# Performance work log

Measured on AMD Instinct MI355X. Metric: run time of the kernel, lower is better.

Reference implementation:

```python
import jax, jax.numpy as jnp
import numpy as np

INP = 512
HIDDEN = 512
N_HEADS = 8          # called 'head_dim' in the torch code
D_HEAD = HIDDEN // N_HEADS  # 64
BASE = 10000.0
SCALE = D_HEAD ** (-0.5)


def rope(x):
    # x: [b, s, h, d]
    b, s, h, d = x.shape
    half = d // 2
    theta = 1.0 / (BASE ** (jnp.arange(0, d, 2, dtype=jnp.float32) / d))  # [d/2]
    idx_theta = jnp.arange(s, dtype=jnp.float32)[:, None] * theta[None, :]  # [s, d/2]
    idx_theta2 = jnp.concatenate([idx_theta, idx_theta], axis=1)            # [s, d]
    neg_half = jnp.concatenate([-x[..., half:], x[..., :half]], axis=-1)
    cos = jnp.cos(idx_theta2)[None, :, None, :]
    sin = jnp.sin(idx_theta2)[None, :, None, :]
    return x * cos + neg_half * sin


def setup_inputs() -> dict:
    key = jax.random.key(0)
    ks = jax.random.split(key, 10)
    b, s = 4, 2048
    init = lambda k, shp, fan_in: jax.random.normal(k, shp, jnp.float32) * (fan_in ** -0.5)
    return {
        "x": jax.random.normal(ks[0], (b, s, INP), jnp.float32),
        "c": jax.random.normal(ks[1], (b, s, INP), jnp.float32),
        "Wq": init(ks[2], (INP, HIDDEN), INP), "bq": jnp.zeros((HIDDEN,), jnp.float32),
        "Wk": init(ks[3], (INP, HIDDEN), INP), "bk": jnp.zeros((HIDDEN,), jnp.float32),
        "Wv": init(ks[4], (INP, HIDDEN), INP), "bv": jnp.zeros((HIDDEN,), jnp.float32),
        "Wo": init(ks[5], (HIDDEN, INP), HIDDEN), "bo": jnp.zeros((INP,), jnp.float32),
    }


def reference(x, c, Wq, bq, Wk, bk, Wv, bv, Wo, bo):
    b, s, _ = x.shape
    h_res = x
    q = (c @ Wq + bq).reshape(b, s, N_HEADS, D_HEAD)
    k = (x @ Wk + bk).reshape(b, s, N_HEADS, D_HEAD)
    v = (x @ Wv + bv).reshape(b, s, N_HEADS, D_HEAD)
    q = rope(q)
    k = rope(k)  # computed but unused, exactly as in the source
    # NOTE: source computes scores between q and V (not k) -- faithful reproduction
    att = jnp.einsum('bihd,bjhd->bhij', q, v)            # [b, h, s, s]
    att = jax.nn.softmax(att * SCALE, axis=-1)
    out = jnp.einsum('bhij,bjhd->bihd', att, v)          # [b, s, h, d]
    out = out.reshape(b, s, HIDDEN)
    out = out @ Wo + bo
    return out + h_res
```

## Files before the change

### kernel.cpp

```cpp
#include <hip/hip_runtime.h>
#include <hip/hip_bf16.h>
#include <cstdint>

typedef float f32x4 __attribute__((ext_vector_type(4)));
typedef float f32x16 __attribute__((ext_vector_type(16)));
typedef short bf16x8 __attribute__((ext_vector_type(8)));
typedef short bf16x4 __attribute__((ext_vector_type(4)));
typedef unsigned int u32x2 __attribute__((ext_vector_type(2)));
typedef unsigned short u16;

#define B_    4
#define S_    2048
#define H_    8
#define D_    64
#define M_    8192

#define OFF_CBF   0UL
#define OFF_XBF   8388608UL
#define OFF_QBH   16777216UL
#define OFF_VBH   25165824UL
#define OFF_VTBH  33554432UL
#define OFF_ATTN  41943040UL
#define OFF_WQT   50331648UL
#define OFF_WVT   50855936UL
#define OFF_WOT   51380224UL
#define OFF_BIAS  51904512UL
#define OFF_COS   51910656UL
#define OFF_SIN   52172800UL
#define WS_NEEDED 52434944UL

__device__ __forceinline__ u16 f2bf(float f){
    union { float f; uint32_t u; } v; v.f = f;
    uint32_t r = (v.u + 0x7fffu + ((v.u >> 16) & 1u)) >> 16;
    return (u16)r;
}
__device__ __forceinline__ float bf2f(u16 h){
    union { uint32_t u; float f; } v; v.u = ((uint32_t)h) << 16;
    return v.f;
}

__device__ __forceinline__ uint32_t cvtpk(float lo, float hi){
    uint32_t r;
    asm("v_cvt_pk_bf16_f32 %0, %1, %2" : "=v"(r) : "v"(lo), "v"(hi));
    return r;
}
__device__ __forceinline__ void plswap(uint32_t &va, uint32_t &vb){
#if __has_builtin(__builtin_amdgcn_permlane32_swap)
    u32x2 r = __builtin_amdgcn_permlane32_swap(va, vb, false, false);
    va = r[0]; vb = r[1];
#else
    asm volatile("v_permlane32_swap_b32 %0, %1" : "+v"(va), "+v"(vb));
#endif
}

__device__ __forceinline__ int swz(int row, int col){
    return (col & ~63) | ((((col >> 3) & 7) ^ (row & 7)) << 3) | (col & 7);
}

__device__ __forceinline__ int detect_f32(const void* x_in){
    int lane = threadIdx.x & 63;
    ushort2 dv = ((const ushort2*)x_in)[lane];
    bool hit = ((((dv.x >> 7) & 0xFF) >= 160) || (((dv.y >> 7) & 0xFF) >= 160));
    return __ballot(hit) != 0ULL;
}

__device__ __forceinline__ void gload_lds16(const u16* g, u16* l){
    __builtin_amdgcn_global_load_lds(
        (const __attribute__((address_space(1))) void*)g,
        (__attribute__((address_space(3))) void*)l, 16, 0, 0);
}

__global__ void k_prep(const void* c_in, const void* x_in,
                       const void* Wq, const void* Wv, const void* Wo,
                       const void* bq, const void* bv, const void* bo,
                       u16* c_bf, u16* x_bf,
                       u16* Wqt, u16* Wvt, u16* Wot, float* bias_ws,
                       float* cos_t, float* sin_t){
    int bid = blockIdx.x;
    if (bid >= 11264){
        int idx = (bid - 11264) * 256 + threadIdx.x;
        int pos = idx >> 5, j = idx & 31;
        double theta = pow(10000.0, -(double)j / 32.0);
        double rev = ((double)pos * theta) * 0.15915494309189535;
        rev -= floor(rev);
        float fr = (float)rev;
        cos_t[idx] = __builtin_amdgcn_cosf(fr);
        sin_t[idx] = __builtin_amdgcn_sinf(fr);
        return;
    }
    if (bid >= 8192){
        int f = detect_f32(x_in);
        int wi = (bid - 8192) >> 10;
        int idx = ((bid - 8192) & 1023) * 256 + threadIdx.x;
        int k = idx >> 9, n = idx & 511;
        const void* W; u16* Wt; const void* bb;
        if (wi == 0){ W = Wq; Wt = Wqt; bb = bq; }
        else if (wi == 1){ W = Wv; Wt = Wvt; bb = bv; }
        else { W = Wo; Wt = Wot; bb = bo; }
        float v = f ? ((const float*)W)[idx] : bf2f(((const u16*)W)[idx]);
        Wt[n * 512 + (wi == 2 ? k : swz(n, k))] = f2bf(v);
        if (idx < 512){
            float b = f ? ((const float*)bb)[idx] : bf2f(((const u16*)bb)[idx]);
            bias_ws[wi * 512 + idx] = b;
        }
        return;
    }
    int f = detect_f32(x_in);
    int isx = bid >= 4096;
    int t = (bid & 4095) * 256 + threadIdx.x;
    const void* src = isx ? x_in : c_in;
    u16* dst = isx ? x_bf : c_bf;
    int e0 = t * 4, row = e0 >> 9, col = e0 & 511;
    size_t didx = (size_t)row * 512 + swz(row, col);
    ushort4 o;
    if (f){
        float4 v = ((const float4*)src)[t];
        o.x = f2bf(v.x); o.y = f2bf(v.y); o.z = f2bf(v.z); o.w = f2bf(v.w);
    } else {
        o = ((const ushort4*)src)[t];
    }
    *(ushort4*)(dst + didx) = o;
}

__global__ __launch_bounds__(256) void k_gemm_qv(
    const u16* __restrict__ c_bf, const u16* __restrict__ x_bf,
    const u16* __restrict__ Wqt, const u16* __restrict__ Wvt,
    const float* __restrict__ bias_ws,
    const float* __restrict__ cos_t, const float* __restrict__ sin_t,
    u16* __restrict__ Qbh, u16* __restrict__ Vbh, u16* __restrict__ Vtbh)
{
    __shared__ __align__(16) u16 Als[2][128 * 64];
    __shared__ __align__(16) u16 Bls[2][128 * 64];
    const int w = threadIdx.x >> 6, lane = threadIdx.x & 63;
    const int g = lane >> 4, cq = lane & 15;
    const int wm = w & 1, wn = w >> 1;
    const int z = blockIdx.z;
    const u16* A  = z ? x_bf : c_bf;
    const u16* Wt = z ? Wvt : Wqt;
    const float* bias = bias_ws + (z ? 512 : 0);
    const int m0b = blockIdx.x * 128, n0b = blockIdx.y * 128;
    const int m0 = m0b + wm * 64, n0 = n0b + wn * 64;
    const int swzi = ((cq & 7) << 3);

    int srow[4], scol[4];
    #pragma unroll
    for (int i = 0; i < 4; i++){
        int flat = (w * 4 + i) * 64 + lane;
        srow[i] = flat >> 3; scol[i] = (flat & 7) * 8;
    }

    const f32x4 zero = {0.f, 0.f, 0.f, 0.f};
    f32x4 acc[4][4];
    #pragma unroll
    for (int i = 0; i < 4; i++)
        #pragma unroll
        for (int j = 0; j < 4; j++) acc[i][j] = zero;

    #pragma unroll
    for (int i = 0; i < 4; i++){
        gload_lds16(A  + (size_t)(m0b + srow[i]) * 512 + scol[i], &Als[0][(w*4 + i) * 512]);
        gload_lds16(Wt + (size_t)(n0b + srow[i]) * 512 + scol[i], &Bls[0][(w*4 + i) * 512]);
    }

    for (int kt = 0; kt < 8; kt++){
        const int buf = kt & 1;
        __builtin_amdgcn_s_waitcnt(0x0F70);
        __syncthreads();
        if (kt < 7){
            const int kk = (kt + 1) * 64;
            #pragma unroll
            for (int i = 0; i < 4; i++){
                gload_lds16(A  + (size_t)(m0b + srow[i]) * 512 + kk + scol[i], &Als[buf^1][(w*4 + i) * 512]);
                gload_lds16(Wt + (size_t)(n0b + srow[i]) * 512 + kk + scol[i], &Bls[buf^1][(w*4 + i) * 512]);
            }
        }
        #pragma unroll
        for (int ks = 0; ks < 2; ks++){
            const int cs = ((ks * 4 + g) << 3) ^ swzi;
            bf16x8 a[4], b[4];
            #pragma unroll
            for (int mt = 0; mt < 4; mt++)
                a[mt] = *(const bf16x8*)&Als[buf][(wm*64 + mt*16 + cq) * 64 + cs];
            #pragma unroll
            for (int nt = 0; nt < 4; nt++)
                b[nt] = *(const bf16x8*)&Bls[buf][(wn*64 + nt*16 + cq) * 64 + cs];
            #pragma unroll
            for (int mt = 0; mt < 4; mt++)
                #pragma unroll
                for (int nt = 0; nt < 4; nt++)
                    acc[mt][nt] = __builtin_amdgcn_mfma_f32_16x16x32_bf16(a[mt], b[nt], acc[mt][nt], 0, 0, 0);
        }
    }
    __syncthreads();

    #pragma unroll
    for (int nt = 0; nt < 4; nt++){
        float bvv = bias[n0 + nt*16 + cq];
        #pragma unroll
        for (int mt = 0; mt < 4; mt++) acc[mt][nt] += bvv;
    }
    const int h = n0 >> 6;
    if (z == 0){
        const float SCL = 0.125f * 1.4426950408889634f;
        #pragma unroll
        for (int mt = 0; mt < 4; mt++){
            #pragma unroll
            for (int r = 0; r < 4; r++){
                int row = m0 + mt*16 + g*4 + r;
                int b_idx = row >> 11, si = row & 2047;
                size_t base = ((size_t)(b_idx*8 + h) * 2048 + si) * 64;
                #pragma unroll
                for (int nt = 0; nt < 2; nt++){
                    int dj = nt*16 + cq;
                    float cv = cos_t[si*32 + dj], sv = sin_t[si*32 + dj];
                    float x1 = acc[mt][nt][r], x2 = acc[mt][nt+2][r];
                    Qbh[base + dj]      = f2bf((x1*cv - x2*sv) * SCL);
                    Qbh[base + dj + 32] = f2bf((x2*cv + x1*sv) * SCL);
                }
            }
        }
    } else {
        float* ltw = ((float*)&Als[0][0]) + w * (16 * 65);
        const int b_idx = m0 >> 11, si0 = m0 & 2047;
        const size_t tbase = ((size_t)(b_idx*8 + h) * 64) * 2048;
        #pragma unroll
        for (int mt = 0; mt < 4; mt++)
            #pragma unroll
            for (int r = 0; r < 4; r++){
                int row = m0 + mt*16 + g*4 + r;
                int bi = row >> 11, si = row & 2047;
                size_t base = ((size_t)(bi*8 + h) * 2048 + si) * 64;
                #pragma unroll
                for (int nt = 0; nt < 4; nt++)
                    Vbh[base + nt*16 + cq] = f2bf(acc[mt][nt][r]);
            }
        #pragma unroll
        for (int nt = 0; nt < 4; nt++){
            #pragma unroll
            for (int mt = 0; mt < 4; mt++)
                #pragma unroll
                for (int r = 0; r < 4; r++)
                    ltw[cq * 65 + mt*16 + g*4 + r] = acc[mt][nt][r];
            __builtin_amdgcn_wave_barrier();
            #pragma unroll
            for (int dd = 0; dd < 16; dd++){
                float v = ltw[dd * 65 + lane];
                Vtbh[tbase + (size_t)(nt*16 + dd) * 2048 + si0 + lane] = f2bf(v);
            }
            __builtin_amdgcn_wave_barrier();
        }
    }
}

__global__ __launch_bounds__(256, 4) void k_attn(
    const u16* __restrict__ Qbh, const u16* __restrict__ Vbh,
    const u16* __restrict__ Vtbh,
    u16* __restrict__ part0, u16* __restrict__ part1, float* __restrict__ lsum)
{
    __shared__ __align__(16) u16 Vs[2][64 * 68];
    __shared__ __align__(16) u16 Vts[2][64 * 68];

    const int bid = blockIdx.x;
    const int logical = (bid & 7) * 128 + (bid >> 3);
    const int xb = logical & 15;
    const int bh = (logical >> 4) & 31;
    const int z  = logical >> 9;

    const int w = threadIdx.x >> 6, lane = threadIdx.x & 63;
    const int r32 = lane & 31, hl = lane >> 5;
    const int i0 = xb * 128 + w * 32;
    const int j0 = z * 1024;

    bf16x8 aq[4];
    #pragma unroll
    for (int kk = 0; kk < 4; kk++)
        aq[kk] = *(const bf16x8*)(Qbh + ((size_t)bh*2048 + i0 + r32)*64 + kk*16 + hl*8);

    const int sr = w * 16 + (lane >> 2), sc = (lane & 3) * 16;
    const u16* gvs = Vbh  + ((size_t)bh*2048 + j0 + sr) * 64 + sc;
    const u16* gvt = Vtbh + ((size_t)bh*64 + sr) * 2048 + j0 + sc;
    const int ls = sr * 68 + sc;

    {
        bf16x8 a0 = *(const bf16x8*)gvs,       a1 = *(const bf16x8*)(gvs + 8);
        bf16x8 b0 = *(const bf16x8*)gvt,       b1 = *(const bf16x8*)(gvt + 8);
        *(bf16x8*)&Vs[0][ls]  = a0;  *(bf16x8*)&Vs[0][ls + 8]  = a1;
        *(bf16x8*)&Vts[0][ls] = b0;  *(bf16x8*)&Vts[0][ls + 8] = b1;
    }

    f32x16 ot0 = {0.f,0.f,0.f,0.f,0.f,0.f,0.f,0.f,0.f,0.f,0.f,0.f,0.f,0.f,0.f,0.f};
    f32x16 ot1 = ot0;
    const f32x16 zero16 = ot0;
    float fl = 0.f;

    for (int jt = 0; jt < 16; jt++){
        const int buf = jt & 1;
        __syncthreads();
        bf16x8 na0, na1, nb0, nb1;
        if (jt < 15){
            na0 = *(const bf16x8*)(gvs + (size_t)(jt + 1) * 4096);
            na1 = *(const bf16x8*)(gvs + (size_t)(jt + 1) * 4096 + 8);
            nb0 = *(const bf16x8*)(gvt + (size_t)(jt + 1) * 64);
            nb1 = *(const bf16x8*)(gvt + (size_t)(jt + 1) * 64 + 8);
        }
        bf16x8 pb[4];
        #pragma unroll
        for (int jtile = 0; jtile < 2; jtile++){
            f32x16 st = zero16;
            __builtin_amdgcn_s_setprio(1);
            #pragma unroll
            for (int kk = 0; kk < 4; kk++){
                bf16x8 av = *(const bf16x8*)&Vs[buf][(jtile*32 + r32)*68 + kk*16 + hl*8];
                st = __builtin_amdgcn_mfma_f32_32x32x16_bf16(av, aq[kk], st, 0, 0, 0);
            }
            __builtin_amdgcn_s_setprio(0);
            #pragma unroll
            for (int rr = 0; rr < 16; rr++) st[rr] = __builtin_amdgcn_exp2f(st[rr]);
            {
                float t0 = (st[0]+st[1]) + (st[2]+st[3]);
                float t1 = (st[4]+st[5]) + (st[6]+st[7]);
                float t2 = (st[8]+st[9]) + (st[10]+st[11]);
                float t3 = (st[12]+st[13]) + (st[14]+st[15]);
                fl += (t0+t1) + (t2+t3);
            }
            #pragma unroll
            for (int c = 0; c < 2; c++){
                uint32_t dA1 = cvtpk(st[c*8+0], st[c*8+1]);
                uint32_t dA2 = cvtpk(st[c*8+2], st[c*8+3]);
                uint32_t dB1 = cvtpk(st[c*8+4], st[c*8+5]);
                uint32_t dB2 = cvtpk(st[c*8+6], st[c*8+7]);
                plswap(dA1, dB1);
                plswap(dA2, dB2);
                union { bf16x8 v; uint32_t d[4]; } u;
                u.d[0] = dA1; u.d[1] = dA2; u.d[2] = dB1; u.d[3] = dB2;
                pb[jtile*2 + c] = u.v;
            }
        }
        __builtin_amdgcn_s_setprio(1);
        #pragma unroll
        for (int c = 0; c < 4; c++){
            bf16x8 vt0 = *(const bf16x8*)&Vts[buf][r32*68 + c*16 + hl*8];
            bf16x8 vt1 = *(const bf16x8*)&Vts[buf][(32 + r32)*68 + c*16 + hl*8];
            ot0 = __builtin_amdgcn_mfma_f32_32x32x16_bf16(vt0, pb[c], ot0, 0, 0, 0);
            ot1 = __builtin_amdgcn_mfma_f32_32x32x16_bf16(vt1, pb[c], ot1, 0, 0, 0);
        }
        __builtin_amdgcn_s_setprio(0);
        if (jt < 15){
            *(bf16x8*)&Vs[buf^1][ls]  = na0;  *(bf16x8*)&Vs[buf^1][ls + 8]  = na1;
            *(bf16x8*)&Vts[buf^1][ls] = nb0;  *(bf16x8*)&Vts[buf^1][ls + 8] = nb1;
        }
    }
    const int b_idx = bh >> 3, hh = bh & 7;
    u16* part = z ? part1 : part0;
    float sum = fl + __shfl_xor(fl, 32);
    const int row = b_idx*2048 + i0 + r32;
    if (lane < 32)
        lsum[(size_t)z*65536 + (size_t)hh*8192 + row] = sum;
    #pragma unroll
    for (int dt = 0; dt < 2; dt++){
        #pragma unroll
        for (int q = 0; q < 4; q++){
            float v0 = dt ? ot1[q*4+0] : ot0[q*4+0];
            float v1 = dt ? ot1[q*4+1] : ot0[q*4+1];
            float v2 = dt ? ot1[q*4+2] : ot0[q*4+2];
            float v3 = dt ? ot1[q*4+3] : ot0[q*4+3];
            uint2 pw;
            pw.x = cvtpk(v0, v1);
            pw.y = cvtpk(v2, v3);
            int col = hh*64 + dt*32 + q*8 + hl*4;
            *(uint2*)&part[(size_t)row * 512 + col] = pw;
        }
    }
}

__global__ __launch_bounds__(256) void k_gemm_out(
    const u16* __restrict__ part0, const u16* __restrict__ part1,
    const float* __restrict__ lsum,
    const u16* __restrict__ Wot, const float* __restrict__ bias_ws,
    const void* __restrict__ x_in, void* __restrict__ out)
{
    __shared__ __align__(16) u16 Als[2][128 * 68];
    __shared__ __align__(16) u16 Bls[2][64 * 68];
    const int w = threadIdx.x >> 6, lane = threadIdx.x & 63;
    const int g = lane >> 4, cq = lane & 15;
    const int wm = w & 1, wn = w >> 1;
    const int m0b = blockIdx.x * 128, n0b = blockIdx.y * 64;
    const int m0 = m0b + wm * 64, n0 = n0b + wn * 32;
    const int f = detect_f32(x_in);

    int sra[4], sca[4], srb[2], scb[2];
    #pragma unroll
    for (int i = 0; i < 4; i++){
        int flat = (w * 4 + i) * 64 + lane;
        sra[i] = flat >> 3; sca[i] = (flat & 7) * 8;
    }
    #pragma unroll
    for (int i = 0; i < 2; i++){
        int flat = (w * 2 + i) * 64 + lane;
        srb[i] = flat >> 3; scb[i] = (flat & 7) * 8;
    }

    const f32x4 zero = {0.f, 0.f, 0.f, 0.f};
    f32x4 acc[4][2];
    #pragma unroll
    for (int i = 0; i < 4; i++)
        #pragma unroll
        for (int j = 0; j < 2; j++) acc[i][j] = zero;

    bf16x8 pa0[4], pa1[4], pb[2]; float pr[4];
    #pragma unroll
    for (int i = 0; i < 4; i++){
        int row = m0b + sra[i];
        pa0[i] = *(const bf16x8*)&part0[(size_t)row * 512 + sca[i]];
        pa1[i] = *(const bf16x8*)&part1[(size_t)row * 512 + sca[i]];
        pr[i] = 1.f / (lsum[row] + lsum[65536 + row]);
    }
    #pragma unroll
    for (int i = 0; i < 2; i++)
        pb[i] = *(const bf16x8*)&Wot[(size_t)(n0b + srb[i]) * 512 + scb[i]];
    #pragma unroll
    for (int i = 0; i < 4; i++){
        union { bf16x8 v; u16 e[8]; } a8;
        #pragma unroll
        for (int e = 0; e < 8; e++)
            a8.e[e] = f2bf((bf2f((u16)pa0[i][e]) + bf2f((u16)pa1[i][e])) * pr[i]);
        *(bf16x8*)&Als[0][sra[i]*68 + sca[i]] = a8.v;
    }
    #pragma unroll
    for (int i = 0; i < 2; i++)
        *(bf16x8*)&Bls[0][srb[i]*68 + scb[i]] = pb[i];

    for (int kt = 0; kt < 8; kt++){
        const int buf = kt & 1;
        __syncthreads();
        if (kt < 7){
            const int kk = (kt + 1) * 64, h = kt + 1;
            #pragma unroll
            for (int i = 0; i < 4; i++){
                int row = m0b + sra[i];
                pa0[i] = *(const bf16x8*)&part0[(size_t)row * 512 + kk + sca[i]];
                pa1[i] = *(const bf16x8*)&part1[(size_t)row * 512 + kk + sca[i]];
                pr[i] = 1.f / (lsum[(size_t)h*8192 + row] + lsum[65536 + (size_t)h*8192 + row]);
            }
            #pragma unroll
            for (int i = 0; i < 2; i++)
                pb[i] = *(const bf16x8*)&Wot[(size_t)(n0b + srb[i]) * 512 + kk + scb[i]];
        }
        #pragma unroll
        for (int ks = 0; ks < 2; ks++){
            bf16x8 a[4], b[2];
            #pragma unroll
            for (int mt = 0; mt < 4; mt++)
                a[mt] = *(const bf16x8*)&Als[buf][(wm*64 + mt*16 + cq)*68 + ks*32 + g*8];
            #pragma unroll
            for (int nt = 0; nt < 2; nt++)
                b[nt] = *(const bf16x8*)&Bls[buf][(wn*32 + nt*16 + cq)*68 + ks*32 + g*8];
            #pragma unroll
            for (int mt = 0; mt < 4; mt++)
                #pragma unroll
                for (int nt = 0; nt < 2; nt++)
                    acc[mt][nt] = __builtin_amdgcn_mfma_f32_16x16x32_bf16(a[mt], b[nt], acc[mt][nt], 0, 0, 0);
        }
        if (kt < 7){
            #pragma unroll
            for (int i = 0; i < 4; i++){
                union { bf16x8 v; u16 e[8]; } a8;
                #pragma unroll
                for (int e = 0; e < 8; e++)
                    a8.e[e] = f2bf((bf2f((u16)pa0[i][e]) + bf2f((u16)pa1[i][e])) * pr[i]);
                *(bf16x8*)&Als[buf^1][sra[i]*68 + sca[i]] = a8.v;
            }
            #pragma unroll
            for (int i = 0; i < 2; i++)
                *(bf16x8*)&Bls[buf^1][srb[i]*68 + scb[i]] = pb[i];
        }
    }
    #pragma unroll
    for (int mt = 0; mt < 4; mt++)
        #pragma unroll
        for (int nt = 0; nt < 2; nt++)
            #pragma unroll
            for (int r = 0; r < 4; r++){
                int row = m0 + mt*16 + g*4 + r;
                int col = n0 + nt*16 + cq;
                size_t idx = (size_t)row * 512 + col;
                float resid = f ? ((const float*)x_in)[idx] : bf2f(((const u16*)x_in)[idx]);
                float v = acc[mt][nt][r] + bias_ws[1024 + col] + resid;
                if (f) ((float*)out)[idx] = v;
                else   ((u16*)out)[idx] = f2bf(v);
            }
}

extern "C" void kernel_launch(void* const* d_in, const int* in_sizes, int n_in,
                              void* d_out, int out_size, void* d_ws, size_t ws_size,
                              hipStream_t stream){
    const void* x_in = d_in[0];
    const void* c_in = d_in[1];
    const void* Wq = d_in[2]; const void* bq = d_in[3];
    const void* Wv = d_in[6]; const void* bv = d_in[7];
    const void* Wo = d_in[8]; const void* bo = d_in[9];

    if (ws_size < WS_NEEDED){
        hipMemsetAsync(d_out, 0, (size_t)out_size * 2, stream);
        return;
    }
    char* ws = (char*)d_ws;
    u16* c_bf  = (u16*)(ws + OFF_CBF);
    u16* x_bf  = (u16*)(ws + OFF_XBF);
    u16* Qbh   = (u16*)(ws + OFF_QBH);
    u16* Vbh   = (u16*)(ws + OFF_VBH);
    u16* Vtbh  = (u16*)(ws + OFF_VTBH);
    u16* part0 = (u16*)(ws + OFF_ATTN);
    u16* part1 = (u16*)(ws + OFF_CBF);
    float* lsum = (float*)(ws + OFF_XBF);
    u16* Wqt   = (u16*)(ws + OFF_WQT);
    u16* Wvt   = (u16*)(ws + OFF_WVT);
    u16* Wot   = (u16*)(ws + OFF_WOT);
    float* bias_ws = (float*)(ws + OFF_BIAS);
    float* cos_t   = (float*)(ws + OFF_COS);
    float* sin_t   = (float*)(ws + OFF_SIN);

    k_prep<<<11520, 256, 0, stream>>>(c_in, x_in, Wq, Wv, Wo, bq, bv, bo,
                                      c_bf, x_bf, Wqt, Wvt, Wot, bias_ws, cos_t, sin_t);
    k_gemm_qv<<<dim3(64, 4, 2), 256, 0, stream>>>(c_bf, x_bf, Wqt, Wvt, bias_ws,
                                                  cos_t, sin_t, Qbh, Vbh, Vtbh);
    k_attn<<<dim3(1024), 256, 0, stream>>>(Qbh, Vbh, Vtbh, part0, part1, lsum);
    k_gemm_out<<<dim3(64, 8), 256, 0, stream>>>(part0, part1, lsum, Wot, bias_ws,
                                                x_in, d_out);
}
```

Before: 188.5 us.

## Process two 32-row query tiles per wave in attention to reuse V tiles

Each wave in the attention kernel now handles 64 query rows (two 32-row MFMA tiles) instead of 32. V fragments loaded from shared memory are reused across both query tiles, which halves LDS reads and global V traffic per unit of work. The grid drops from 1024 to 512 blocks and the occupancy hint goes from 4 to 2 blocks per CU, so register pressure rises and there is less parallelism to hide latency.

```diff
diff --git a/kernel.cpp b/kernel.cpp
--- a/kernel.cpp
+++ b/kernel.cpp
@@ -252,7 +252,7 @@
     }
 }
 
-__global__ __launch_bounds__(256, 4) void k_attn(
+__global__ __launch_bounds__(256, 2) void k_attn(
     const u16* __restrict__ Qbh, const u16* __restrict__ Vbh,
     const u16* __restrict__ Vtbh,
     u16* __restrict__ part0, u16* __restrict__ part1, float* __restrict__ lsum)
@@ -261,20 +261,22 @@
     __shared__ __align__(16) u16 Vts[2][64 * 68];
 
     const int bid = blockIdx.x;
-    const int logical = (bid & 7) * 128 + (bid >> 3);
-    const int xb = logical & 15;
-    const int bh = (logical >> 4) & 31;
-    const int z  = logical >> 9;
+    const int logical = (bid & 7) * 64 + (bid >> 3);
+    const int xb = logical & 7;
+    const int bh = (logical >> 3) & 31;
+    const int z  = logical >> 8;
 
     const int w = threadIdx.x >> 6, lane = threadIdx.x & 63;
     const int r32 = lane & 31, hl = lane >> 5;
-    const int i0 = xb * 128 + w * 32;
+    const int i0 = xb * 256 + w * 64;
     const int j0 = z * 1024;
 
-    bf16x8 aq[4];
-    #pragma unroll
-    for (int kk = 0; kk < 4; kk++)
-        aq[kk] = *(const bf16x8*)(Qbh + ((size_t)bh*2048 + i0 + r32)*64 + kk*16 + hl*8);
+    bf16x8 aq[2][4];
+    #pragma unroll
+    for (int it = 0; it < 2; it++)
+        #pragma unroll
+        for (int kk = 0; kk < 4; kk++)
+            aq[it][kk] = *(const bf16x8*)(Qbh + ((size_t)bh*2048 + i0 + it*32 + r32)*64 + kk*16 + hl*8);
 
     const int sr = w * 16 + (lane >> 2), sc = (lane & 3) * 16;
     const u16* gvs = Vbh  + ((size_t)bh*2048 + j0 + sr) * 64 + sc;
@@ -288,10 +290,15 @@
         *(bf16x8*)&Vts[0][ls] = b0;  *(bf16x8*)&Vts[0][ls + 8] = b1;
     }
 
-    f32x16 ot0 = {0.f,0.f,0.f,0.f,0.f,0.f,0.f,0.f,0.f,0.f,0.f,0.f,0.f,0.f,0.f,0.f};
-    f32x16 ot1 = ot0;
-    const f32x16 zero16 = ot0;
-    float fl = 0.f;
+    f32x16 ot[2][2];
+    #pragma unroll
+    for (int it = 0; it < 2; it++)
+        #pragma unroll
+        for (int dt = 0; dt < 2; dt++)
+            #pragma unroll
+            for (int rr = 0; rr < 16; rr++) ot[it][dt][rr] = 0.f;
+    const f32x16 zero16 = ot[0][0];
+    float fl[2] = {0.f, 0.f};
 
     for (int jt = 0; jt < 16; jt++){
         const int buf = jt & 1;
@@ -303,37 +310,60 @@
             nb0 = *(const bf16x8*)(gvt + (size_t)(jt + 1) * 64);
             nb1 = *(const bf16x8*)(gvt + (size_t)(jt + 1) * 64 + 8);
         }
-        bf16x8 pb[4];
+        bf16x8 pb[2][4];
         #pragma unroll
         for (int jtile = 0; jtile < 2; jtile++){
-            f32x16 st = zero16;
+            bf16x8 vf[4];
+            #pragma unroll
+            for (int kk = 0; kk < 4; kk++)
+                vf[kk] = *(const bf16x8*)&Vs[buf][(jtile*32 + r32)*68 + kk*16 + hl*8];
+            f32x16 st0 = zero16, st1 = zero16;
             __builtin_amdgcn_s_setprio(1);
             #pragma unroll
             for (int kk = 0; kk < 4; kk++){
-                bf16x8 av = *(const bf16x8*)&Vs[buf][(jtile*32 + r32)*68 + kk*16 + hl*8];
-                st = __builtin_amdgcn_mfma_f32_32x32x16_bf16(av, aq[kk], st, 0, 0, 0);
+                st0 = __builtin_amdgcn_mfma_f32_32x32x16_bf16(vf[kk], aq[0][kk], st0, 0, 0, 0);
+                st1 = __builtin_amdgcn_mfma_f32_32x32x16_bf16(vf[kk], aq[1][kk], st1, 0, 0, 0);
             }
             __builtin_amdgcn_s_setprio(0);
             #pragma unroll
-            for (int rr = 0; rr < 16; rr++) st[rr] = __builtin_amdgcn_exp2f(st[rr]);
+            for (int rr = 0; rr < 16; rr++) st0[rr] = __builtin_amdgcn_exp2f(st0[rr]);
+            #pragma unroll
+            for (int rr = 0; rr < 16; rr++) st1[rr] = __builtin_amdgcn_exp2f(st1[rr]);
             {
-                float t0 = (st[0]+st[1]) + (st[2]+st[3]);
-                float t1 = (st[4]+st[5]) + (st[6]+st[7]);
-                float t2 = (st[8]+st[9]) + (st[10]+st[11]);
-                float t3 = (st[12]+st[13]) + (st[14]+st[15]);
-                fl += (t0+t1) + (t2+t3);
+                float a0 = (st0[0]+st0[1]) + (st0[2]+st0[3]);
+                float a1 = (st0[4]+st0[5]) + (st0[6]+st0[7]);
+                float a2 = (st0[8]+st0[9]) + (st0[10]+st0[11]);
+                float a3 = (st0[12]+st0[13]) + (st0[14]+st0[15]);
+                fl[0] += (a0+a1) + (a2+a3);
+                float b0 = (st1[0]+st1[1]) + (st1[2]+st1[3]);
+                float b1 = (st1[4]+st1[5]) + (st1[6]+st1[7]);
+                float b2 = (st1[8]+st1[9]) + (st1[10]+st1[11]);
+                float b3 = (st1[12]+st1[13]) + (st1[14]+st1[15]);
+                fl[1] += (b0+b1) + (b2+b3);
             }
             #pragma unroll
             for (int c = 0; c < 2; c++){
-                uint32_t dA1 = cvtpk(st[c*8+0], st[c*8+1]);
-                uint32_t dA2 = cvtpk(st[c*8+2], st[c*8+3]);
-                uint32_t dB1 = cvtpk(st[c*8+4], st[c*8+5]);
-                uint32_t dB2 = cvtpk(st[c*8+6], st[c*8+7]);
+                uint32_t dA1 = cvtpk(st0[c*8+0], st0[c*8+1]);
+                uint32_t dA2 = cvtpk(st0[c*8+2], st0[c*8+3]);
+                uint32_t dB1 = cvtpk(st0[c*8+4], st0[c*8+5]);
+                uint32_t dB2 = cvtpk(st0[c*8+6], st0[c*8+7]);
                 plswap(dA1, dB1);
                 plswap(dA2, dB2);
                 union { bf16x8 v; uint32_t d[4]; } u;
                 u.d[0] = dA1; u.d[1] = dA2; u.d[2] = dB1; u.d[3] = dB2;
-                pb[jtile*2 + c] = u.v;
+                pb[0][jtile*2 + c] = u.v;
+            }
+            #pragma unroll
+            for (int c = 0; c < 2; c++){
+                uint32_t dA1 = cvtpk(st1[c*8+0], st1[c*8+1]);
+                uint32_t dA2 = cvtpk(st1[c*8+2], st1[c*8+3]);
+                uint32_t dB1 = cvtpk(st1[c*8+4], st1[c*8+5]);
+                uint32_t dB2 = cvtpk(st1[c*8+6], st1[c*8+7]);
+                plswap(dA1, dB1);
+                plswap(dA2, dB2);
+                union { bf16x8 v; uint32_t d[4]; } u;
+                u.d[0] = dA1; u.d[1] = dA2; u.d[2] = dB1; u.d[3] = dB2;
+                pb[1][jtile*2 + c] = u.v;
             }
         }
         __builtin_amdgcn_s_setprio(1);
@@ -341,8 +371,10 @@
         for (int c = 0; c < 4; c++){
             bf16x8 vt0 = *(const bf16x8*)&Vts[buf][r32*68 + c*16 + hl*8];
             bf16x8 vt1 = *(const bf16x8*)&Vts[buf][(32 + r32)*68 + c*16 + hl*8];
-            ot0 = __builtin_amdgcn_mfma_f32_32x32x16_bf16(vt0, pb[c], ot0, 0, 0, 0);
-            ot1 = __builtin_amdgcn_mfma_f32_32x32x16_bf16(vt1, pb[c], ot1, 0, 0, 0);
+            ot[0][0] = __builtin_amdgcn_mfma_f32_32x32x16_bf16(vt0, pb[0][c], ot[0][0], 0, 0, 0);
+            ot[1][0] = __builtin_amdgcn_mfma_f32_32x32x16_bf16(vt0, pb[1][c], ot[1][0], 0, 0, 0);
+            ot[0][1] = __builtin_amdgcn_mfma_f32_32x32x16_bf16(vt1, pb[0][c], ot[0][1], 0, 0, 0);
+            ot[1][1] = __builtin_amdgcn_mfma_f32_32x32x16_bf16(vt1, pb[1][c], ot[1][1], 0, 0, 0);
         }
         __builtin_amdgcn_s_setprio(0);
         if (jt < 15){
@@ -352,23 +384,26 @@
     }
     const int b_idx = bh >> 3, hh = bh & 7;
     u16* part = z ? part1 : part0;
-    float sum = fl + __shfl_xor(fl, 32);
-    const int row = b_idx*2048 + i0 + r32;
-    if (lane < 32)
-        lsum[(size_t)z*65536 + (size_t)hh*8192 + row] = sum;
-    #pragma unroll
-    for (int dt = 0; dt < 2; dt++){
-        #pragma unroll
-        for (int q = 0; q < 4; q++){
-            float v0 = dt ? ot1[q*4+0] : ot0[q*4+0];
-            float v1 = dt ? ot1[q*4+1] : ot0[q*4+1];
-            float v2 = dt ? ot1[q*4+2] : ot0[q*4+2];
-            float v3 = dt ? ot1[q*4+3] : ot0[q*4+3];
-            uint2 pw;
-            pw.x = cvtpk(v0, v1);
-            pw.y = cvtpk(v2, v3);
-            int col = hh*64 + dt*32 + q*8 + hl*4;
-            *(uint2*)&part[(size_t)row * 512 + col] = pw;
+    #pragma unroll
+    for (int it = 0; it < 2; it++){
+        float sum = fl[it] + __shfl_xor(fl[it], 32);
+        const int row = b_idx*2048 + i0 + it*32 + r32;
+        if (lane < 32)
+            lsum[(size_t)z*65536 + (size_t)hh*8192 + row] = sum;
+        #pragma unroll
+        for (int dt = 0; dt < 2; dt++){
+            #pragma unroll
+            for (int q = 0; q < 4; q++){
+                float v0 = ot[it][dt][q*4+0];
+                float v1 = ot[it][dt][q*4+1];
+                float v2 = ot[it][dt][q*4+2];
+                float v3 = ot[it][dt][q*4+3];
+                uint2 pw;
+                pw.x = cvtpk(v0, v1);
+                pw.y = cvtpk(v2, v3);
+                int col = hh*64 + dt*32 + q*8 + hl*4;
+                *(uint2*)&part[(size_t)row * 512 + col] = pw;
+            }
         }
     }
 }
@@ -524,7 +559,7 @@
                                       c_bf, x_bf, Wqt, Wvt, Wot, bias_ws, cos_t, sin_t);
     k_gemm_qv<<<dim3(64, 4, 2), 256, 0, stream>>>(c_bf, x_bf, Wqt, Wvt, bias_ws,
                                                   cos_t, sin_t, Qbh, Vbh, Vtbh);
-    k_attn<<<dim3(1024), 256, 0, stream>>>(Qbh, Vbh, Vtbh, part0, part1, lsum);
+    k_attn<<<dim3(512), 256, 0, stream>>>(Qbh, Vbh, Vtbh, part0, part1, lsum);
     k_gemm_out<<<dim3(64, 8), 256, 0, stream>>>(part0, part1, lsum, Wot, bias_ws,
                                                 x_in, d_out);
 }
```

Measured after the change: 182.0 us. 3.5% less time.
